# Optimization experiments

Measured on AMD Instinct MI355X. Metric: run time of the kernel, lower is better.

Reference implementation:

```python
import jax, jax.numpy as jnp
import numpy as np

B = 4096
C3 = 1.0 / np.sqrt(3.0)
# Wigner 3j tensors for the l<=1 paths (e3nn real basis)
W3J_000 = jnp.ones((1, 1, 1), dtype=jnp.float32)
W3J_110 = (jnp.eye(3) * C3).reshape(3, 3, 1).astype(jnp.float32)
W3J_011 = (jnp.eye(3) * C3).reshape(1, 3, 3).astype(jnp.float32)
W3J_101 = (jnp.eye(3) * C3).reshape(3, 1, 3).astype(jnp.float32)


def setup_inputs() -> dict:
    key = jax.random.key(0)
    ks = jax.random.split(key, 10)
    n = lambda k, s: jax.random.normal(k, s, dtype=jnp.float32)
    return {
        "feat": n(ks[0], (B, 320)),        # 128x0e + 64x1o
        "node_emb": n(ks[1], (B, 128)),
        # o3.Linear(irreps_node -> irreps_block): one mixing matrix per l
        "W0": n(ks[2], (128, 16)),          # 0e: 128 -> 16
        "W1": n(ks[3], (64, 16)),           # 1o: 64 -> 16
        # lin_weight MLP: 128 -> 64 -> 36864
        "lw1": n(ks[4], (128, 64)) * 0.1, "lb1": jnp.zeros((64,), jnp.float32),
        "lw2": n(ks[5], (64, 36864)) * 0.1, "lb2": jnp.zeros((36864,), jnp.float32),
        # lin_bias MLP: 128 -> 64 -> 1280
        "bw1": n(ks[6], (128, 64)) * 0.1, "bb1": jnp.zeros((64,), jnp.float32),
        "bw2": n(ks[7], (64, 1280)) * 0.1, "bb2": jnp.zeros((1280,), jnp.float32),
    }


def _path(x, wpath, w3j, bias):
    # x: [B, mul_in, dim_in]; wpath: [B, mul_in, u, v]; w3j: [i, j, k]
    r = jnp.einsum('bwuv,bwk->buvk', wpath, x)
    if bias is not None:
        r = r + bias[..., None]
    out = jnp.einsum('ijk,buvk->buivj', w3j, r) / x.shape[1]
    b, u, i, v, j = out.shape
    return out.reshape(b, u * i, v * j)


def reference(feat, node_emb, W0, W1, lw1, lb1, lw2, lb2, bw1, bb1, bw2, bb2):
    bn = feat.shape[0]
    # split feat into irreps: 128x0e | 64x1o
    s = feat[:, :128].reshape(bn, 128, 1)
    v = feat[:, 128:].reshape(bn, 64, 3)
    # o3.Linear with e3nn path normalization 1/sqrt(fan_in)
    x0 = jnp.einsum('buk,uv->bvk', s, W0) / np.sqrt(128.0)  # [B,16,1]
    x1 = jnp.einsum('buk,uv->bvk', v, W1) / np.sqrt(64.0)   # [B,16,3]
    # per-sample path weights and biases
    w = jax.nn.silu(node_emb @ lw1 + lb1) @ lw2 + lb2        # [B,36864]
    bb = jax.nn.silu(node_emb @ bw1 + bb1) @ bw2 + bb2       # [B,1280]
    # weight slices per instruction (flat layout matches instruction order)
    w00 = w[:, :16384].reshape(bn, 16, 32, 32)               # 0e -> (0e,0e)
    w11 = w[:, 16384:20480].reshape(bn, 16, 16, 16)          # 0e -> (1o,1o)
    w01 = w[:, 20480:28672].reshape(bn, 16, 32, 16)          # 1o -> (0e,1o)
    w10 = w[:, 28672:36864].reshape(bn, 16, 16, 32)          # 1o -> (1o,0e)
    b00 = bb[:, :1024].reshape(bn, 32, 32)
    b11 = bb[:, 1024:1280].reshape(bn, 16, 16)
    blk00 = _path(x0, w00, W3J_000, b00)   # [B,32,32]
    blk11 = _path(x0, w11, W3J_110, b11)   # [B,48,48]
    blk01 = _path(x1, w01, W3J_011, None)  # [B,32,48]
    blk10 = _path(x1, w10, W3J_101, None)  # [B,48,32]
    top = jnp.concatenate([blk00, blk01], axis=-1)
    bot = jnp.concatenate([blk10, blk11], axis=-1)
    return jnp.concatenate([top, bot], axis=-2)  # [B,80,80]
```

## Files before the change

### kernel.cpp

```cpp
#include <hip/hip_runtime.h>
#include <hip/hip_bf16.h>
#include <math.h>


typedef short bf16x8 __attribute__((ext_vector_type(8)));
typedef float f32x4 __attribute__((ext_vector_type(4)));

static __device__ __forceinline__ short f2bf(float f) {
  unsigned u = __builtin_bit_cast(unsigned, f);
  u = u + 0x7fffu + ((u >> 16) & 1u);
  return (short)(u >> 16);
}

__global__ void k_transpose(const float* __restrict__ lw2, short* __restrict__ lw2f) {
  __shared__ float tile[64][65];
  int n0 = blockIdx.x * 64;
  int t = threadIdx.x;
#pragma unroll
  for (int k = 0; k < 16; ++k) {
    int idx = k * 256 + t;
    int c = idx >> 6, j = idx & 63;
    tile[c][j] = lw2[(size_t)c * 36864 + n0 + j];
  }
  __syncthreads();
#pragma unroll
  for (int k = 0; k < 16; ++k) {
    int idx = k * 256 + t;
    int e = idx & 7, l = (idx >> 3) & 63, half = (idx >> 9) & 1, nbl = idx >> 10;
    int q = l >> 4, colr = l & 15;
    int j = nbl * 16 + colr;
    int c = half * 32 + q * 8 + e;
    size_t nb = (size_t)(n0 >> 4) + nbl;
    lw2f[((nb * 2 + half) * 64 + l) * 8 + e] = f2bf(tile[c][j]);
  }
}

__global__ void k_bias(const float* __restrict__ bw2, const float* __restrict__ lb2,
                       const float* __restrict__ bb2,
                       short* __restrict__ bbf00, short* __restrict__ bbf11,
                       short* __restrict__ bbf01, short* __restrict__ bbf10) {
  int i = blockIdx.x * 256 + threadIdx.x;
  if (i < 98304) {
    int uvb = i / 1536, r = i % 1536;
    int kk = r >> 9, l = (r >> 3) & 63, e = r & 7;
    int q = l >> 4, col = l & 15;
    int uv = uvb * 16 + col, k = kk * 32 + q * 8 + e;
    float v = 0.0f;
    if (k < 64) v = bw2[k * 1280 + uv];
    else if (k < 80) v = lb2[(k - 64) * 1024 + uv];
    else if (k == 80) v = bb2[uv];
    bbf00[i] = f2bf(v);
  } else if (i < 122880) {
    int j = i - 98304;
    int uvb = j / 1536, r = j % 1536;
    int kk = r >> 9, l = (r >> 3) & 63, e = r & 7;
    int q = l >> 4, col = l & 15;
    int uv = uvb * 16 + col, k = kk * 32 + q * 8 + e;
    float v = 0.0f;
    if (k < 64) v = bw2[k * 1280 + 1024 + uv];
    else if (k < 80) v = lb2[16384 + (k - 64) * 256 + uv];
    else if (k == 80) v = bb2[1024 + uv];
    bbf11[j] = f2bf(v);
  } else if (i < 139264) {
    int j = i - 122880;
    int uvb = j >> 9, r = j & 511;
    int l = (r >> 3) & 63, e = r & 7;
    int q = l >> 4, col = l & 15;
    int uv = uvb * 16 + col, k = q * 8 + e;
    bbf01[j] = (k < 16) ? f2bf(lb2[20480 + k * 512 + uv]) : (short)0;
  } else if (i < 155648) {
    int j = i - 139264;
    int uvb = j >> 9, r = j & 511;
    int l = (r >> 3) & 63, e = r & 7;
    int q = l >> 4, col = l & 15;
    int uv = uvb * 16 + col, k = q * 8 + e;
    bbf10[j] = (k < 16) ? f2bf(lb2[28672 + k * 512 + uv]) : (short)0;
  }
}

__global__ void k_samples(const float* __restrict__ feat, const float* __restrict__ ne,
                          const float* __restrict__ W0, const float* __restrict__ W1,
                          const float* __restrict__ lw1, const float* __restrict__ lb1,
                          const float* __restrict__ bw1, const float* __restrict__ bb1,
                          float* __restrict__ H, float* __restrict__ H2,
                          float* __restrict__ X0, float* __restrict__ X1) {
  int b = blockIdx.x;
  int t = threadIdx.x;
  __shared__ float sne[128];
  __shared__ float sf[320];
  if (t < 128) sne[t] = ne[(size_t)b * 128 + t];
  for (int i = t; i < 320; i += 192) sf[i] = feat[(size_t)b * 320 + i];
  __syncthreads();
  if (t < 64) {
    float a = lb1[t];
    for (int k = 0; k < 128; ++k) a += sne[k] * lw1[k * 64 + t];
    H[(size_t)b * 64 + t] = a / (1.0f + expf(-a));
  } else if (t < 128) {
    int c = t - 64;
    float a = bb1[c];
    for (int k = 0; k < 128; ++k) a += sne[k] * bw1[k * 64 + c];
    H2[(size_t)b * 64 + c] = a / (1.0f + expf(-a));
  } else if (t < 144) {
    int v = t - 128;
    float a = 0.0f;
    for (int u = 0; u < 128; ++u) a += sf[u] * W0[u * 16 + v];
    X0[(size_t)b * 16 + v] = a * 0.08838834764831845f;
  } else {
    int idx = t - 144, v = idx / 3, j = idx % 3;
    float a = 0.0f;
    for (int u = 0; u < 64; ++u) a += sf[128 + u * 3 + j] * W1[u * 16 + v];
    X1[(size_t)b * 48 + v * 3 + j] = a * 0.125f;
  }
}

__global__ void k_q(const float* __restrict__ H, const float* __restrict__ H2,
                    const float* __restrict__ X0, const float* __restrict__ X1,
                    short* __restrict__ QF, short* __restrict__ AbF,
                    short* __restrict__ A1F) {
  int bid = blockIdx.x;
  int g16 = bid >> 3, part = bid & 7;
  int b0 = g16 * 16;
  int t = threadIdx.x;
  __shared__ float sH[16][64];
  __shared__ float sH2[16][64];
  __shared__ float sX0[16][16];
  __shared__ float sX1[16][48];
  for (int i = t; i < 1024; i += 256) {
    sH [i >> 6][i & 63] = H [(size_t)(b0 + (i >> 6)) * 64 + (i & 63)];
    sH2[i >> 6][i & 63] = H2[(size_t)(b0 + (i >> 6)) * 64 + (i & 63)];
  }
  sX0[t >> 4][t & 15] = X0[(size_t)(b0 + (t >> 4)) * 16 + (t & 15)];
  for (int i = t; i < 768; i += 256)
    sX1[i / 48][i % 48] = X1[(size_t)(b0 + i / 48) * 48 + (i % 48)];
  __syncthreads();
#pragma unroll
  for (int it = 0; it < 16; ++it) {
    int i = part * 4096 + it * 256 + t;
    int p = i >> 13, rem = i & 8191;
    int kk = rem >> 8, lane = (rem >> 2) & 63, e2 = (rem & 3) << 1;
    int cc = lane & 15, q = lane >> 4;
    int k = kk * 32 + q * 8 + e2;
    int w = k >> 6, c = k & 63;
    float xw = (p == 0) ? sX0[cc][w] : sX1[cc][w * 3 + (p - 1)];
    unsigned lo = (unsigned short)f2bf(sH[cc][c] * xw);
    unsigned hi = (unsigned short)f2bf(sH[cc][c + 1] * xw);
    ((unsigned*)QF)[(size_t)g16 * 32768 + i] = lo | (hi << 16);
  }
  if (part == 0) {
    for (int i = t; i < 1536; i += 256) {
      int kk = i >> 9, lane = (i >> 3) & 63, e = i & 7;
      int cc = lane & 15, q = lane >> 4;
      int k = kk * 32 + q * 8 + e;
      float v = 0.0f;
      if (k < 64) v = sH2[cc][k];
      else if (k < 80) v = sX0[cc][k - 64];
      else if (k == 80) v = 1.0f;
      AbF[(size_t)g16 * 1536 + i] = f2bf(v);
    }
  } else if (part == 1) {
    for (int i = t; i < 1536; i += 256) {
      int j = i >> 9, r = i & 511;
      int lane = r >> 3, e = r & 7;
      int cc = lane & 15, q = lane >> 4;
      int k = q * 8 + e;
      A1F[(size_t)g16 * 1536 + i] = (k < 16) ? f2bf(sX1[cc][k * 3 + j]) : (short)0;
    }
  }
}

template <int NP, int N, int NB16, int NS16>
static __device__ __forceinline__ void mm_stream(
    const short* __restrict__ LW2F, const short* __restrict__ sQ0,
    int uvb, int lane8, f32x4 (&acc)[NP][N]) {
  auto bptr = [&](int kk, int i) -> const bf16x8* {
    return (const bf16x8*)(LW2F +
        ((size_t)(NB16 + (kk >> 1) * NS16 + uvb + i) * 2 + (kk & 1)) * 512 + lane8);
  };
  bf16x8 B[2][N];
#pragma unroll
  for (int d = 0; d < 2; ++d)
#pragma unroll
    for (int i = 0; i < N; ++i) B[d][i] = *bptr(d, i);
#pragma unroll
  for (int kk = 0; kk < 32; ++kk) {
    const int d = kk & 1;
    bf16x8 A[NP];
#pragma unroll
    for (int p = 0; p < NP; ++p)
      A[p] = *(const bf16x8*)(sQ0 + p * 16384 + kk * 512 + lane8);
#pragma unroll
    for (int i = 0; i < N; ++i)
#pragma unroll
      for (int p = 0; p < NP; ++p)
        acc[p][i] = __builtin_amdgcn_mfma_f32_16x16x32_bf16(A[p], B[d][i], acc[p][i], 0, 0, 0);
    if (kk + 2 < 32) {
#pragma unroll
      for (int i = 0; i < N; ++i) B[d][i] = *bptr(kk + 2, i);
    }
  }
}

template <int NP, int N, int NBIAS>
static __device__ __forceinline__ void mm_bias(
    const short* __restrict__ BBF, const short* __restrict__ Ab0, int astride,
    int uvb, int lane8, f32x4 (&acc)[NP][N]) {
#pragma unroll
  for (int kk = 0; kk < NBIAS; ++kk)
#pragma unroll
    for (int i = 0; i < N; ++i) {
      const bf16x8 Bx = *(const bf16x8*)(BBF + (size_t)((uvb + i) * NBIAS + kk) * 512 + lane8);
#pragma unroll
      for (int p = 0; p < NP; ++p) {
        const bf16x8 Ap = *(const bf16x8*)(Ab0 + p * astride + kk * 512 + lane8);
        acc[p][i] = __builtin_amdgcn_mfma_f32_16x16x32_bf16(Ap, Bx, acc[p][i], 0, 0, 0);
      }
    }
}

__global__ __launch_bounds__(512, 1) void k_main(
    const short* __restrict__ LW2F,
    const short* __restrict__ BBF00, const short* __restrict__ BBF11,
    const short* __restrict__ BBF01, const short* __restrict__ BBF10,
    const short* __restrict__ QF, const short* __restrict__ AbF,
    const short* __restrict__ A1F, float* __restrict__ out) {
  constexpr float S00 = 0.0625f;
  constexpr float S3 = 0.036084391824351614f;

  int bidx = blockIdx.x;
  int xslot = bidx & 7;
  int h = xslot >> 2;
  int tile = (xslot & 3) + 4 * (bidx >> 3);
  int b0 = tile << 4;
  int t = threadIdx.x;
  int lane = t & 63, slot = t >> 6;
  int col = lane & 15, q = lane >> 4;
  int lane8 = lane * 8;

  __shared__ short sQ[2 * 16384];
  __shared__ short sAb[1536];
  __shared__ short sA1[1536];

  for (int i = t; i < 2048; i += 512)
    ((uint4*)sQ)[i] = ((const uint4*)(QF + (size_t)tile * 65536))[i];
  if (t < 192) ((uint4*)sAb)[t] = ((const uint4*)(AbF + (size_t)tile * 1536))[t];
  else if (t < 384)
    ((uint4*)sA1)[t - 192] = ((const uint4*)(A1F + (size_t)tile * 1536))[t - 192];
  __syncthreads();

#pragma unroll 1
  for (int pp = 0; pp < 2; ++pp) {
    int uvb = h * 32 + slot * 4 + pp * 2;
    f32x4 acc[1][2] = {};
    mm_stream<1, 2, 0, 64>(LW2F, sQ, uvb, lane8, acc);
    mm_bias<1, 2, 3>(BBF00, sAb, 1536, uvb, lane8, acc);
#pragma unroll
    for (int i = 0; i < 2; ++i)
#pragma unroll
      for (int ii = 0; ii < 4; ++ii) {
        size_t ob = (size_t)(b0 + q * 4 + ii) * 6400;
        int uv = (uvb + i) * 16 + col;
        out[ob + (uv >> 5) * 80 + (uv & 31)] = acc[0][i][ii] * S00;
      }
  }
  {
    int uvb = h * 8 + slot;
    f32x4 acc[1][1] = {};
    mm_stream<1, 1, 1024, 16>(LW2F, sQ, uvb, lane8, acc);
    mm_bias<1, 1, 3>(BBF11, sAb, 1536, uvb, lane8, acc);
#pragma unroll
    for (int ii = 0; ii < 4; ++ii) {
      size_t ob = (size_t)(b0 + q * 4 + ii) * 6400;
      int uv = uvb * 16 + col;
      float val = acc[0][0][ii] * S3;
      int u = uv >> 4, v = uv & 15;
      float* p = out + ob + (size_t)(32 + 3 * u) * 80 + (32 + 3 * v);
      p[0] = val;   p[1] = 0.f;   p[2] = 0.f;
      p[80] = 0.f;  p[81] = val;  p[82] = 0.f;
      p[160] = 0.f; p[161] = 0.f; p[162] = val;
    }
  }

  __syncthreads();
  for (int i = t; i < 4096; i += 512) {
    int pl = i >> 11, r = i & 2047;
    ((uint4*)sQ)[i] = ((const uint4*)(QF + ((size_t)tile * 4 + 1 + pl) * 16384))[r];
  }
  __syncthreads();
  {
    int uvb = h * 16 + slot * 2;
    {
      f32x4 acc[2][2] = {};
      mm_stream<2, 2, 1280, 32>(LW2F, sQ, uvb, lane8, acc);
      mm_bias<2, 2, 1>(BBF01, sA1, 512, uvb, lane8, acc);
#pragma unroll
      for (int p = 0; p < 2; ++p)
#pragma unroll
        for (int i = 0; i < 2; ++i)
#pragma unroll
          for (int ii = 0; ii < 4; ++ii) {
            size_t ob = (size_t)(b0 + q * 4 + ii) * 6400;
            int uv = (uvb + i) * 16 + col;
            out[ob + (uv >> 4) * 80 + 32 + 3 * (uv & 15) + p] = acc[p][i][ii] * S3;
          }
    }
    {
      f32x4 acc[2][2] = {};
      mm_stream<2, 2, 1792, 32>(LW2F, sQ, uvb, lane8, acc);
      mm_bias<2, 2, 1>(BBF10, sA1, 512, uvb, lane8, acc);
#pragma unroll
      for (int p = 0; p < 2; ++p)
#pragma unroll
        for (int i = 0; i < 2; ++i)
#pragma unroll
          for (int ii = 0; ii < 4; ++ii) {
            size_t ob = (size_t)(b0 + q * 4 + ii) * 6400;
            int uv = (uvb + i) * 16 + col;
            out[ob + (size_t)(32 + 3 * (uv >> 5) + p) * 80 + (uv & 31)] = acc[p][i][ii] * S3;
          }
    }
  }

  __syncthreads();
  for (int i = t; i < 2048; i += 512)
    ((uint4*)sQ)[i] = ((const uint4*)(QF + ((size_t)tile * 4 + 3) * 16384))[i];
  __syncthreads();
  {
    int uvb = h * 16 + slot * 2;
    {
      f32x4 acc[1][2] = {};
      mm_stream<1, 2, 1280, 32>(LW2F, sQ, uvb, lane8, acc);
      mm_bias<1, 2, 1>(BBF01, sA1 + 1024, 512, uvb, lane8, acc);
#pragma unroll
      for (int i = 0; i < 2; ++i)
#pragma unroll
        for (int ii = 0; ii < 4; ++ii) {
          size_t ob = (size_t)(b0 + q * 4 + ii) * 6400;
          int uv = (uvb + i) * 16 + col;
          out[ob + (uv >> 4) * 80 + 32 + 3 * (uv & 15) + 2] = acc[0][i][ii] * S3;
        }
    }
    {
      f32x4 acc[1][2] = {};
      mm_stream<1, 2, 1792, 32>(LW2F, sQ, uvb, lane8, acc);
      mm_bias<1, 2, 1>(BBF10, sA1 + 1024, 512, uvb, lane8, acc);
#pragma unroll
      for (int i = 0; i < 2; ++i)
#pragma unroll
        for (int ii = 0; ii < 4; ++ii) {
          size_t ob = (size_t)(b0 + q * 4 + ii) * 6400;
          int uv = (uvb + i) * 16 + col;
          out[ob + (size_t)(32 + 3 * (uv >> 5) + 2) * 80 + (uv & 31)] = acc[0][i][ii] * S3;
        }
    }
  }
}

extern "C" void kernel_launch(void* const* d_in, const int* in_sizes, int n_in,
                              void* d_out, int out_size, void* d_ws, size_t ws_size,
                              hipStream_t stream) {
  const float* feat = (const float*)d_in[0];
  const float* ne   = (const float*)d_in[1];
  const float* W0   = (const float*)d_in[2];
  const float* W1   = (const float*)d_in[3];
  const float* lw1  = (const float*)d_in[4];
  const float* lb1  = (const float*)d_in[5];
  const float* lw2  = (const float*)d_in[6];
  const float* lb2  = (const float*)d_in[7];
  const float* bw1  = (const float*)d_in[8];
  const float* bb1  = (const float*)d_in[9];
  const float* bw2  = (const float*)d_in[10];
  const float* bb2  = (const float*)d_in[11];

  char* ws = (char*)d_ws;
  short* LW2F  = (short*)ws; ws += (size_t)36864 * 64 * 2;
  short* BBF00 = (short*)ws; ws += (size_t)98304 * 2;
  short* BBF11 = (short*)ws; ws += (size_t)24576 * 2;
  short* BBF01 = (short*)ws; ws += (size_t)16384 * 2;
  short* BBF10 = (short*)ws; ws += (size_t)16384 * 2;
  float* H  = (float*)ws;   ws += (size_t)4096 * 64 * 4;
  float* H2 = (float*)ws;   ws += (size_t)4096 * 64 * 4;
  float* X0 = (float*)ws;   ws += (size_t)4096 * 16 * 4;
  float* X1 = (float*)ws;   ws += (size_t)4096 * 48 * 4;
  short* QF  = (short*)ws;  ws += (size_t)256 * 65536 * 2;
  short* AbF = (short*)ws;  ws += (size_t)256 * 1536 * 2;
  short* A1F = (short*)ws;  ws += (size_t)256 * 1536 * 2;
  (void)ws_size; (void)in_sizes; (void)n_in; (void)out_size;

  hipLaunchKernelGGL(k_transpose, dim3(576), dim3(256), 0, stream, lw2, LW2F);
  hipLaunchKernelGGL(k_bias, dim3(608), dim3(256), 0, stream, bw2, lb2, bb2,
                     BBF00, BBF11, BBF01, BBF10);
  hipLaunchKernelGGL(k_samples, dim3(4096), dim3(192), 0, stream,
                     feat, ne, W0, W1, lw1, lb1, bw1, bb1, H, H2, X0, X1);
  hipLaunchKernelGGL(k_q, dim3(2048), dim3(256), 0, stream,
                     H, H2, X0, X1, QF, AbF, A1F);
  hipLaunchKernelGGL(k_main, dim3(512), dim3(512), 0, stream,
                     LW2F, BBF00, BBF11, BBF01, BBF10, QF, AbF, A1F, (float*)d_out);
}
```

Before: 170.9 us.

## Halve shared Q buffer and defer all output stores to a single epilogue

Shrinks the shared Q staging buffer from two planes to one by processing the three vector components in a loop, one plane at a time. All path results are kept in registers (r00, r11, r01, r10) and written to the output in one final epilogue grouped by output row. The intent is lower LDS usage for more resident blocks, plus more clustered global writes. The cost is extra synchronisations and LW2F streaming passes for the l=1 paths, which are now done per component instead of two at once, and higher register pressure from holding every accumulator until the end.

```diff
diff --git a/kernel.cpp b/kernel.cpp
--- a/kernel.cpp
+++ b/kernel.cpp
@@ -236,7 +236,7 @@
   int col = lane & 15, q = lane >> 4;
   int lane8 = lane * 8;
 
-  __shared__ short sQ[2 * 16384];
+  __shared__ short sQ[16384];
   __shared__ short sAb[1536];
   __shared__ short sA1[1536];
 
@@ -247,111 +247,78 @@
     ((uint4*)sA1)[t - 192] = ((const uint4*)(A1F + (size_t)tile * 1536))[t - 192];
   __syncthreads();
 
-#pragma unroll 1
+  f32x4 r00[2][2];
+  f32x4 r11;
+  f32x4 r01[3][2];
+  f32x4 r10[3][2];
+
+#pragma unroll
   for (int pp = 0; pp < 2; ++pp) {
     int uvb = h * 32 + slot * 4 + pp * 2;
     f32x4 acc[1][2] = {};
     mm_stream<1, 2, 0, 64>(LW2F, sQ, uvb, lane8, acc);
     mm_bias<1, 2, 3>(BBF00, sAb, 1536, uvb, lane8, acc);
-#pragma unroll
-    for (int i = 0; i < 2; ++i)
-#pragma unroll
-      for (int ii = 0; ii < 4; ++ii) {
-        size_t ob = (size_t)(b0 + q * 4 + ii) * 6400;
-        int uv = (uvb + i) * 16 + col;
-        out[ob + (uv >> 5) * 80 + (uv & 31)] = acc[0][i][ii] * S00;
-      }
+    r00[pp][0] = acc[0][0] * S00;
+    r00[pp][1] = acc[0][1] * S00;
   }
   {
     int uvb = h * 8 + slot;
     f32x4 acc[1][1] = {};
     mm_stream<1, 1, 1024, 16>(LW2F, sQ, uvb, lane8, acc);
     mm_bias<1, 1, 3>(BBF11, sAb, 1536, uvb, lane8, acc);
-#pragma unroll
-    for (int ii = 0; ii < 4; ++ii) {
-      size_t ob = (size_t)(b0 + q * 4 + ii) * 6400;
-      int uv = uvb * 16 + col;
-      float val = acc[0][0][ii] * S3;
+    r11 = acc[0][0] * S3;
+  }
+
+#pragma unroll
+  for (int j = 0; j < 3; ++j) {
+    __syncthreads();
+    for (int i = t; i < 2048; i += 512)
+      ((uint4*)sQ)[i] = ((const uint4*)(QF + ((size_t)tile * 4 + 1 + j) * 16384))[i];
+    __syncthreads();
+    int uvb = h * 16 + slot * 2;
+    {
+      f32x4 acc[1][2] = {};
+      mm_stream<1, 2, 1280, 32>(LW2F, sQ, uvb, lane8, acc);
+      mm_bias<1, 2, 1>(BBF01, sA1 + j * 512, 512, uvb, lane8, acc);
+      r01[j][0] = acc[0][0] * S3;
+      r01[j][1] = acc[0][1] * S3;
+    }
+    {
+      f32x4 acc[1][2] = {};
+      mm_stream<1, 2, 1792, 32>(LW2F, sQ, uvb, lane8, acc);
+      mm_bias<1, 2, 1>(BBF10, sA1 + j * 512, 512, uvb, lane8, acc);
+      r10[j][0] = acc[0][0] * S3;
+      r10[j][1] = acc[0][1] * S3;
+    }
+  }
+
+#pragma unroll
+  for (int ii = 0; ii < 4; ++ii) {
+    size_t ob = (size_t)(b0 + q * 4 + ii) * 6400;
+#pragma unroll
+    for (int pp = 0; pp < 2; ++pp)
+#pragma unroll
+      for (int i = 0; i < 2; ++i) {
+        int uv = (h * 32 + slot * 4 + pp * 2 + i) * 16 + col;
+        out[ob + (uv >> 5) * 80 + (uv & 31)] = r00[pp][i][ii];
+      }
+    {
+      int uv = (h * 8 + slot) * 16 + col;
+      float val = r11[ii];
       int u = uv >> 4, v = uv & 15;
       float* p = out + ob + (size_t)(32 + 3 * u) * 80 + (32 + 3 * v);
       p[0] = val;   p[1] = 0.f;   p[2] = 0.f;
       p[80] = 0.f;  p[81] = val;  p[82] = 0.f;
       p[160] = 0.f; p[161] = 0.f; p[162] = val;
     }
-  }
-
-  __syncthreads();
-  for (int i = t; i < 4096; i += 512) {
-    int pl = i >> 11, r = i & 2047;
-    ((uint4*)sQ)[i] = ((const uint4*)(QF + ((size_t)tile * 4 + 1 + pl) * 16384))[r];
-  }
-  __syncthreads();
-  {
-    int uvb = h * 16 + slot * 2;
-    {
-      f32x4 acc[2][2] = {};
-      mm_stream<2, 2, 1280, 32>(LW2F, sQ, uvb, lane8, acc);
-      mm_bias<2, 2, 1>(BBF01, sA1, 512, uvb, lane8, acc);
-#pragma unroll
-      for (int p = 0; p < 2; ++p)
-#pragma unroll
-        for (int i = 0; i < 2; ++i)
-#pragma unroll
-          for (int ii = 0; ii < 4; ++ii) {
-            size_t ob = (size_t)(b0 + q * 4 + ii) * 6400;
-            int uv = (uvb + i) * 16 + col;
-            out[ob + (uv >> 4) * 80 + 32 + 3 * (uv & 15) + p] = acc[p][i][ii] * S3;
-          }
-    }
-    {
-      f32x4 acc[2][2] = {};
-      mm_stream<2, 2, 1792, 32>(LW2F, sQ, uvb, lane8, acc);
-      mm_bias<2, 2, 1>(BBF10, sA1, 512, uvb, lane8, acc);
-#pragma unroll
-      for (int p = 0; p < 2; ++p)
-#pragma unroll
-        for (int i = 0; i < 2; ++i)
-#pragma unroll
-          for (int ii = 0; ii < 4; ++ii) {
-            size_t ob = (size_t)(b0 + q * 4 + ii) * 6400;
-            int uv = (uvb + i) * 16 + col;
-            out[ob + (size_t)(32 + 3 * (uv >> 5) + p) * 80 + (uv & 31)] = acc[p][i][ii] * S3;
-          }
-    }
-  }
-
-  __syncthreads();
-  for (int i = t; i < 2048; i += 512)
-    ((uint4*)sQ)[i] = ((const uint4*)(QF + ((size_t)tile * 4 + 3) * 16384))[i];
-  __syncthreads();
-  {
-    int uvb = h * 16 + slot * 2;
-    {
-      f32x4 acc[1][2] = {};
-      mm_stream<1, 2, 1280, 32>(LW2F, sQ, uvb, lane8, acc);
-      mm_bias<1, 2, 1>(BBF01, sA1 + 1024, 512, uvb, lane8, acc);
-#pragma unroll
-      for (int i = 0; i < 2; ++i)
-#pragma unroll
-        for (int ii = 0; ii < 4; ++ii) {
-          size_t ob = (size_t)(b0 + q * 4 + ii) * 6400;
-          int uv = (uvb + i) * 16 + col;
-          out[ob + (uv >> 4) * 80 + 32 + 3 * (uv & 15) + 2] = acc[0][i][ii] * S3;
-        }
-    }
-    {
-      f32x4 acc[1][2] = {};
-      mm_stream<1, 2, 1792, 32>(LW2F, sQ, uvb, lane8, acc);
-      mm_bias<1, 2, 1>(BBF10, sA1 + 1024, 512, uvb, lane8, acc);
-#pragma unroll
-      for (int i = 0; i < 2; ++i)
-#pragma unroll
-        for (int ii = 0; ii < 4; ++ii) {
-          size_t ob = (size_t)(b0 + q * 4 + ii) * 6400;
-          int uv = (uvb + i) * 16 + col;
-          out[ob + (size_t)(32 + 3 * (uv >> 5) + 2) * 80 + (uv & 31)] = acc[0][i][ii] * S3;
-        }
-    }
+#pragma unroll
+    for (int j = 0; j < 3; ++j)
+#pragma unroll
+      for (int i = 0; i < 2; ++i) {
+        int uv = (h * 16 + slot * 2 + i) * 16 + col;
+        out[ob + (uv >> 4) * 80 + 32 + 3 * (uv & 15) + j] = r01[j][i][ii];
+        out[ob + (size_t)(32 + 3 * (uv >> 5) + j) * 80 + (uv & 31)] = r10[j][i][ii];
+      }
   }
 }
 
```

Measured after the change: 380.4 us. 123% more time.
